# Performance work log

Measured on AMD Instinct MI355X. Metric: run time of the kernel, lower is better.

Reference implementation:

```python
import jax, jax.numpy as jnp
import numpy as np

N, IN_DIM, D, H, E_DIM, G, NPG = 512, 16, 256, 8, 6, 32, 16
C = D           # per-head channels in GATv2Conv/TransformerConv (out_channels=d_model)
HD = D // H     # MultiheadAttention head dim


def _ln(x, g, b, eps=1e-5):
    m = jnp.mean(x, -1, keepdims=True)
    v = jnp.mean((x - m) ** 2, -1, keepdims=True)
    return (x - m) * jax.lax.rsqrt(v + eps) * g + b


def _seg_softmax(logits, seg, n):
    # numerically stable softmax over edges grouped by destination node
    m = jax.ops.segment_max(logits, seg, num_segments=n)
    m = jnp.where(jnp.isfinite(m), m, 0.0)
    e = jnp.exp(logits - m[seg])
    s = jax.ops.segment_sum(e, seg, num_segments=n)
    return e / jnp.maximum(s[seg], 1e-16)


def _forward(x, edge_attr, emb_w, emb_b, emb_g, emb_bb, pe, gat_lw, gat_lb, gat_rw, gat_rb, gat_ew, gat_att, gat_bias, tq_w, tq_b, tk_w, tk_b, tv_w, tv_b, te_w, tskip_w, tskip_b, tbeta_w, ln_g, ln_b, mha_in_w, mha_in_b, mha_out_w, mha_out_b, pool_w, pool_b, c1_w, c1_b, c1_g, c1_bb, rb_w, rb_b, rb_g, rb_bb, c2_w, c2_b, edge_index, batch):
    src, dst = edge_index[0], edge_index[1]
    E = edge_attr.shape[0]
    # input embedding (Linear + LayerNorm) + learned positional encoding (eval: no dropout)
    h = _ln(x @ emb_w.T + emb_b, emb_g, emb_bb) + pe[:N]
    residual = h
    # --- GATv2Conv(d_model, d_model, heads=H, edge_dim=6, concat=False, add_self_loops=False) ---
    xl = (h @ gat_lw.T + gat_lb).reshape(N, H, C)          # source transform
    xr = (h @ gat_rw.T + gat_rb).reshape(N, H, C)          # target transform
    ee = (edge_attr @ gat_ew.T).reshape(E, H, C)
    z = jax.nn.leaky_relu(xl[src] + xr[dst] + ee, 0.2)
    a = _seg_softmax(jnp.einsum('ehc,hc->eh', z, gat_att), dst, N)
    x_gat = jax.ops.segment_sum(xl[src] * a[..., None], dst, num_segments=N).mean(1) + gat_bias
    x_gat = _ln(x_gat, ln_g, ln_b)
    # --- TransformerConv(d_model, d_model, heads=H, edge_dim=6, concat=False, beta=True) ---
    te = (edge_attr @ te_w.T).reshape(E, H, C)
    q = (x_gat @ tq_w.T + tq_b).reshape(N, H, C)[dst]
    k = (x_gat @ tk_w.T + tk_b).reshape(N, H, C)[src] + te
    v = (x_gat @ tv_w.T + tv_b).reshape(N, H, C)[src] + te
    a2 = _seg_softmax((q * k).sum(-1) / np.sqrt(C).astype(np.float32), dst, N)
    out = jax.ops.segment_sum(v * a2[..., None], dst, num_segments=N).mean(1)
    r = x_gat @ tskip_w.T + tskip_b
    beta = jax.nn.sigmoid(jnp.concatenate([out, r, out - r], -1) @ tbeta_w.T)
    x_tr = _ln(beta * r + (1.0 - beta) * out, ln_g, ln_b)
    # --- dynamic attention mask: after the repeat/permute/reshape gymnastics this equals
    #     ds[:N] repeated H*N times, reshaped to [H, N, N] ---
    im = edge_attr[:, 5]
    ds = jnp.exp(-0.5 * ((im - 125.09) / 15.0) ** 2)
    ds = 1.0 - (ds - ds.min()) / (ds.max() - ds.min())
    mask = jnp.repeat(ds[:N], H * N).reshape(H, N, N)
    # --- cross MultiheadAttention (query=x_tr, key=x_gat, value=h, attn_mask added) ---
    wq, wk, wv = jnp.split(mha_in_w, 3, axis=0)
    bq, bk, bv = jnp.split(mha_in_b, 3, axis=0)
    qh = ((x_tr @ wq.T + bq) / np.sqrt(HD).astype(np.float32)).reshape(N, H, HD).transpose(1, 0, 2)
    kh = (x_gat @ wk.T + bk).reshape(N, H, HD).transpose(1, 0, 2)
    vh = (h @ wv.T + bv).reshape(N, H, HD).transpose(1, 0, 2)
    attn = jax.nn.softmax(qh @ kh.transpose(0, 2, 1) + mask, axis=-1)   # [H,N,N]
    o = (attn @ vh).transpose(1, 0, 2).reshape(N, D) @ mha_out_w.T + mha_out_b
    # torch broadcast of [N,1,D] attn output + [N,D] residual -> [N,N,D]
    x3 = o[:, None, :] + residual[None, :, :]
    # attention pooling: softmax over a size-1 dim yields all-ones scores (kept faithfully)
    x2 = x3.reshape(N * N, D)
    brep = jnp.tile(batch, N)
    score = jax.nn.softmax(x2 @ pool_w.T + pool_b, axis=1)
    pooled = jax.ops.segment_sum(score * x2, brep, num_segments=G)
    # classifier: Linear->LN->GELU->ResidualBlockv2->Linear (dropout off in eval)
    c = jax.nn.gelu(_ln(pooled @ c1_w.T + c1_b, c1_g, c1_bb), approximate=False)
    c = c + jax.nn.gelu(_ln(c @ rb_w.T + rb_b, rb_g, rb_bb), approximate=False)
    return c @ c2_w.T + c2_b   # [G, 1]


def setup_inputs():
    key = jax.random.key(0)
    ks = iter(jax.random.split(key, 64))
    f = lambda *sh: 0.02 * jax.random.normal(next(ks), sh, jnp.float32)
    # G fully-connected directed cliques of NPG nodes (no self loops) -> every node has in-edges
    i = np.arange(NPG)
    s, t = np.meshgrid(i, i, indexing='ij')
    msk = s != t
    s, t = s[msk], t[msk]
    off = (np.arange(G) * NPG)[:, None]
    edge_index = jnp.asarray(np.stack([(s[None] + off).reshape(-1), (t[None] + off).reshape(-1)]), jnp.int32)
    E = edge_index.shape[1]
    batch = jnp.asarray(np.repeat(np.arange(G), NPG), jnp.int32)
    x = jax.random.normal(next(ks), (N, IN_DIM), jnp.float32)
    edge_attr = jax.random.normal(next(ks), (E, E_DIM), jnp.float32)
    edge_attr = edge_attr.at[:, 5].set(edge_attr[:, 5] * 30.0 + 125.0)  # invariant-mass-like column
    HC = H * C
    return dict(
        x=x, edge_attr=edge_attr,
        emb_w=f(D, IN_DIM), emb_b=f(D), emb_g=jnp.ones(D), emb_bb=jnp.zeros(D),
        pe=f(1000, D),
        gat_lw=f(HC, D), gat_lb=f(HC), gat_rw=f(HC, D), gat_rb=f(HC),
        gat_ew=f(HC, E_DIM), gat_att=f(H, C), gat_bias=f(C),
        tq_w=f(HC, D), tq_b=f(HC), tk_w=f(HC, D), tk_b=f(HC),
        tv_w=f(HC, D), tv_b=f(HC), te_w=f(HC, E_DIM),
        tskip_w=f(D, D), tskip_b=f(D), tbeta_w=f(1, 3 * D),
        ln_g=jnp.ones(D), ln_b=jnp.zeros(D),
        mha_in_w=f(3 * D, D), mha_in_b=f(3 * D), mha_out_w=f(D, D), mha_out_b=f(D),
        pool_w=f(1, D), pool_b=f(1),
        c1_w=f(128, D), c1_b=f(128), c1_g=jnp.ones(128), c1_bb=jnp.zeros(128),
        rb_w=f(128, 128), rb_b=f(128), rb_g=jnp.ones(128), rb_bb=jnp.zeros(128),
        c2_w=f(1, 128), c2_b=f(1),
        edge_index=edge_index, batch=batch)


def reference(x, edge_attr, emb_w, emb_b, emb_g, emb_bb, pe, gat_lw, gat_lb, gat_rw, gat_rb, gat_ew, gat_att, gat_bias, tq_w, tq_b, tk_w, tk_b, tv_w, tv_b, te_w, tskip_w, tskip_b, tbeta_w, ln_g, ln_b, mha_in_w, mha_in_b, mha_out_w, mha_out_b, pool_w, pool_b, c1_w, c1_b, c1_g, c1_bb, rb_w, rb_b, rb_g, rb_bb, c2_w, c2_b, edge_index, batch):
    return _forward(x, edge_attr, emb_w, emb_b, emb_g, emb_bb, pe, gat_lw, gat_lb, gat_rw, gat_rb, gat_ew, gat_att, gat_bias, tq_w, tq_b, tk_w, tk_b, tv_w, tv_b, te_w, tskip_w, tskip_b, tbeta_w, ln_g, ln_b, mha_in_w, mha_in_b, mha_out_w, mha_out_b, pool_w, pool_b, c1_w, c1_b, c1_g, c1_bb, rb_w, rb_b, rb_g, rb_bb, c2_w, c2_b, edge_index, batch)
```

## Files before the change

kernel.cpp:

```cpp
#include <hip/hip_runtime.h>
#include <hip/hip_bf16.h>
#include <math.h>

#define NN 512
#define DM 256
#define NH 8
#define NG 32
#define NPG 16
#define INDIM 16
#define BIGW (2048 * 256)
#define WT_SKIP 0
#define WT_MHA  65536
#define WT_OUT  (65536 + 196608)
#define WT_TOTAL (65536 + 196608 + 65536)

typedef __hip_bfloat16 bf16;
typedef __attribute__((ext_vector_type(8))) short short8;
typedef __attribute__((ext_vector_type(4))) float f32x4;

__device__ __forceinline__ float b2f(bf16 v) { return __bfloat162float(v); }
__device__ __forceinline__ bf16 f2b(float v) { return __float2bfloat16(v); }
__device__ __forceinline__ short f2bs(float v) { bf16 t = __float2bfloat16(v); return *(short*)&t; }
__device__ __forceinline__ float fin(float v) {
    return (v == v && v > -1e30f && v < 1e30f) ? v : 0.f;
}
__device__ __forceinline__ int is_bf16(const void* ones_arr) {
    return ((const unsigned short*)ones_arr)[0] == 0x3F80u;
}
__device__ __forceinline__ float ldv(const void* p, size_t i, int bf) {
    return bf ? b2f(((const bf16*)p)[i]) : ((const float*)p)[i];
}

__device__ __forceinline__ void unpack8(uint4 u, float* w) {
    unsigned uu[4] = {u.x, u.y, u.z, u.w};
    #pragma unroll
    for (int j = 0; j < 4; j++) {
        __hip_bfloat162 b2 = *reinterpret_cast<const __hip_bfloat162*>(&uu[j]);
        float2 f = __bfloat1622float2(b2);
        w[2 * j] = f.x; w[2 * j + 1] = f.y;
    }
}
__device__ __forceinline__ float4 bload4(const bf16* p) {
    uint2 u = *(const uint2*)p;
    __hip_bfloat162 a = *reinterpret_cast<const __hip_bfloat162*>(&u.x);
    __hip_bfloat162 b = *reinterpret_cast<const __hip_bfloat162*>(&u.y);
    float2 f0 = __bfloat1622float2(a), f1 = __bfloat1622float2(b);
    return make_float4(f0.x, f0.y, f1.x, f1.y);
}

__device__ __forceinline__ float dot256(const float* xrow, const bf16* wrow) {
    const uint4* w4 = (const uint4*)wrow;
    uint4 q = w4[0];
    float acc = 0.f;
    for (int k8 = 0; k8 < 32; k8++) {
        uint4 qn = w4[(k8 + 1) & 31];
        float w[8]; unpack8(q, w);
        const float4* sp = (const float4*)&xrow[k8 * 8];
        float4 a0 = sp[0], a1 = sp[1];
        acc += a0.x*w[0] + a0.y*w[1] + a0.z*w[2] + a0.w*w[3]
             + a1.x*w[4] + a1.y*w[5] + a1.z*w[6] + a1.w*w[7];
        q = qn;
    }
    return acc;
}

__device__ __forceinline__ float dot256T(const float* xrow, const bf16* wt, int r) {
    float acc = 0.f;
    #pragma unroll 8
    for (int k4 = 0; k4 < 64; k4++) {
        uint2 u = *(const uint2*)(wt + ((size_t)k4 * 256 + r) * 4);
        __hip_bfloat162 b0 = *reinterpret_cast<const __hip_bfloat162*>(&u.x);
        __hip_bfloat162 b1 = *reinterpret_cast<const __hip_bfloat162*>(&u.y);
        float2 f0 = __bfloat1622float2(b0), f1 = __bfloat1622float2(b1);
        float4 xv = *(const float4*)&xrow[k4 * 4];
        acc += xv.x * f0.x + xv.y * f0.y + xv.z * f1.x + xv.w * f1.y;
    }
    return acc;
}

template<int BS>
__device__ __forceinline__ float ln_norm(float v, float g, float b, float* red) {
    int t = threadIdx.x;
    red[t] = v; __syncthreads();
    for (int s = BS / 2; s > 0; s >>= 1) { if (t < s) red[t] += red[t + s]; __syncthreads(); }
    float mean = red[0] * (1.0f / (float)BS); __syncthreads();
    float d = v - mean;
    red[t] = d * d; __syncthreads();
    for (int s = BS / 2; s > 0; s >>= 1) { if (t < s) red[t] += red[t + s]; __syncthreads(); }
    float var = red[0] * (1.0f / (float)BS); __syncthreads();
    return d * rsqrtf(var + 1e-5f) * g + b;
}

struct CvtTab { const void* p[35]; int cum[36]; };
struct Cvt5 { const void* p[5]; };
__global__ void k_convert_all(Cvt5 tab5, CvtTab tab, const void* ones, bf16* wbig,
                              bf16* wbuf, float* gz, int nz, bf16* wt,
                              float* pre1, float* pre2, float* h) {
    int i = blockIdx.x * 256 + threadIdx.x;
    int a = blockIdx.y;
    int bf = is_bf16(ones);
    if (a < 5) {
        if (i >= BIGW) return;
        float v = bf ? b2f(((const bf16*)tab5.p[a])[i]) : ((const float*)tab5.p[a])[i];
        int row = i >> 8, k = i & 255;
        int hh = row >> 8, col = row & 255;
        int T = col >> 4, n16 = col & 15;
        int ks = k >> 5, quad = (k >> 3) & 3, j = k & 7;
        int dst = ((((hh * 16 + T) * 8 + ks) * 4 + quad) * 16 + n16) * 8 + j;
        wbig[(size_t)a * BIGW + dst] = f2b(v);
    } else if (a == 5) {
        if (i < tab.cum[35]) {
            int aa = 0;
            while (i >= tab.cum[aa + 1]) aa++;
            wbuf[i] = f2b(ldv(tab.p[aa], i - tab.cum[aa], bf));
        } else if (i < tab.cum[35] + nz) {
            gz[i - tab.cum[35]] = 0.f;
        } else if (i < tab.cum[35] + nz + WT_TOTAL) {
            int off = i - tab.cum[35] - nz;
            if (off < 65536) {
                int row = off >> 8, k = off & 255;
                wt[WT_SKIP + ((k >> 2) * 256 + row) * 4 + (k & 3)] =
                    f2b(ldv(tab.p[16], off, bf));
            } else if (off < 65536 + 196608) {
                int o2 = off - 65536;
                int row = o2 >> 8, k = o2 & 255;
                int which = row >> 8, r = row & 255;
                wt[WT_MHA + which * 65536 + ((k >> 2) * 256 + r) * 4 + (k & 3)] =
                    f2b(ldv(tab.p[21], o2, bf));
            } else {
                int o2 = off - 65536 - 196608;
                int row = o2 >> 8, k = o2 & 255;
                wt[WT_OUT + ((k >> 2) * 256 + row) * 4 + (k & 3)] =
                    f2b(ldv(tab.p[23], o2, bf));
            }
        }
    } else {
        int n = blockIdx.x;
        if (n >= NN) return;
        int t = threadIdx.x;
        size_t gi = (size_t)n * DM + t;
        pre1[gi] = 0.f;
        pre2[gi] = 0.f;
        __shared__ float xin[INDIM];
        __shared__ float red[DM];
        if (t < INDIM) xin[t] = ldv(tab.p[0], n * INDIM + t, bf);
        __syncthreads();
        float acc = ldv(tab.p[3], t, bf);
        #pragma unroll
        for (int k = 0; k < INDIM; k++) acc += xin[k] * ldv(tab.p[2], t * INDIM + k, bf);
        float y = ln_norm<DM>(acc, ldv(tab.p[4], t, bf), ldv(tab.p[5], t, bf), red);
        h[gi] = fin(y + ldv(tab.p[6], gi, bf));
    }
}

__device__ __forceinline__ void row_softmax16(float* M, int tid) {
    if (tid < NPG) {
        float* row = M + tid * NPG;
        float m = -1e30f;
        #pragma unroll
        for (int s = 0; s < NPG; s++) m = fmaxf(m, row[s]);
        if (m < -1e29f) {
            #pragma unroll
            for (int s = 0; s < NPG; s++) row[s] = 0.f;
        } else {
            float sum = 0.f;
            #pragma unroll
            for (int s = 0; s < NPG; s++) sum += expf(row[s] - m);
            float inv = 1.f / fmaxf(sum, 1e-16f);
            #pragma unroll
            for (int s = 0; s < NPG; s++) row[s] = expf(row[s] - m) * inv;
        }
    }
}

__global__ __launch_bounds__(512, 1)
void k_gat_fused(const float* h, const bf16* lw, const bf16* rw,
                 const bf16* lb, const bf16* rbv, const bf16* eww, const bf16* attw,
                 const bf16* ea, const int* src, const int* dst, int epg, float* pre) {
    extern __shared__ char smraw[];
    int g = blockIdx.x, hh = blockIdx.y, tid = threadIdx.x;
    bf16* hb     = (bf16*)smraw;
    bf16* ew_s   = hb + NPG * DM;
    bf16* att_s  = ew_s + 6 * DM;
    float* ea_s  = (float*)(att_s + DM);
    float* Mx    = ea_s + 6 * epg;
    int* sl_s    = (int*)(Mx + NPG * NPG);
    int* dl_s    = sl_s + epg;
    bf16* xl_s   = (bf16*)(dl_s + epg);
    bf16* xr_s   = xl_s + NPG * DM;

    int ebase = g * epg;
    for (int i = tid; i < NPG * DM; i += 512) hb[i] = f2b(h[(size_t)g * NPG * DM + i]);
    for (int i = tid; i < 6 * DM; i += 512) {
        int f = i >> 8, cc = i & 255;
        ew_s[f * DM + cc] = eww[(size_t)(hh * DM + cc) * 6 + f];
    }
    if (tid < DM) att_s[tid] = attw[hh * DM + tid];
    for (int i = tid; i < 6 * epg; i += 512) {
        int f = i / epg, e = i - f * epg;
        ea_s[f * epg + e] = b2f(ea[(size_t)(ebase + e) * 6 + f]);
    }
    if (tid < NPG * NPG) Mx[tid] = -1e30f;
    if (tid < epg) {
        int e = ebase + tid;
        sl_s[tid] = (src[e] - g * NPG) & (NPG - 1);
        dl_s[tid] = (dst[e] - g * NPG) & (NPG - 1);
    }
    __syncthreads();

    int lane = tid & 63, wave = tid >> 6;
    int n16 = lane & 15, quad = lane >> 4;
    f32x4 accA[2], accB[2];
    #pragma unroll
    for (int ct = 0; ct < 2; ct++) { accA[ct] = (f32x4)0.f; accB[ct] = (f32x4)0.f; }
    for (int ks = 0; ks < 8; ks++) {
        short8 a8 = *(const short8*)&hb[n16 * DM + ks * 32 + quad * 8];
        #pragma unroll
        for (int ct = 0; ct < 2; ct++) {
            int T = ct * 8 + wave;
            size_t fo = (((size_t)(hh * 16 + T) * 8 + ks) * 4 + quad) * 128 + n16 * 8;
            short8 bL = *(const short8*)(lw + fo);
            short8 bR = *(const short8*)(rw + fo);
            accA[ct] = __builtin_amdgcn_mfma_f32_16x16x32_bf16(a8, bL, accA[ct], 0, 0, 0);
            accB[ct] = __builtin_amdgcn_mfma_f32_16x16x32_bf16(a8, bR, accB[ct], 0, 0, 0);
        }
    }
    #pragma unroll
    for (int ct = 0; ct < 2; ct++) {
        int col = (ct * 8 + wave) * 16 + n16;
        float blv = b2f(lb[hh * DM + col]), brv = b2f(rbv[hh * DM + col]);
        #pragma unroll
        for (int reg = 0; reg < 4; reg++) {
            int row = quad * 4 + reg;
            xl_s[row * DM + col] = f2b(accA[ct][reg] + blv);
            xr_s[row * DM + col] = f2b(accB[ct][reg] + brv);
        }
    }
    __syncthreads();

    int c4 = lane * 4;
    for (int ei = wave; ei < epg; ei += 8) {
        int sl = sl_s[ei], dl = dl_s[ei];
        float ee0 = 0.f, ee1 = 0.f, ee2 = 0.f, ee3 = 0.f;
        #pragma unroll
        for (int f = 0; f < 6; f++) {
            float eb = ea_s[f * epg + ei];
            float4 wf = bload4(&ew_s[f * DM + c4]);
            ee0 += eb * wf.x; ee1 += eb * wf.y; ee2 += eb * wf.z; ee3 += eb * wf.w;
        }
        float4 av = bload4(&att_s[c4]);
        float4 xlv = bload4(&xl_s[sl * DM + c4]);
        float4 xrv = bload4(&xr_s[dl * DM + c4]);
        float z0 = xlv.x + xrv.x + ee0;
        float z1 = xlv.y + xrv.y + ee1;
        float z2 = xlv.z + xrv.z + ee2;
        float z3 = xlv.w + xrv.w + ee3;
        z0 = (z0 >= 0.f) ? z0 : 0.2f * z0;
        z1 = (z1 >= 0.f) ? z1 : 0.2f * z1;
        z2 = (z2 >= 0.f) ? z2 : 0.2f * z2;
        z3 = (z3 >= 0.f) ? z3 : 0.2f * z3;
        float acc = z0 * av.x + z1 * av.y + z2 * av.z + z3 * av.w;
        #pragma unroll
        for (int off = 32; off > 0; off >>= 1) acc += __shfl_down(acc, off);
        if (lane == 0) Mx[dl * NPG + sl] = fin(acc);
    }
    __syncthreads();
    row_softmax16(Mx, tid);
    __syncthreads();

    int c = tid & 255, halfd = tid >> 8;
    float xlv[NPG];
    #pragma unroll
    for (int s = 0; s < NPG; s++) xlv[s] = b2f(xl_s[s * DM + c]);
    #pragma unroll
    for (int dd = 0; dd < 8; dd++) {
        int d = halfd * 8 + dd;
        const float* Ar = Mx + d * NPG;
        float acc = 0.f;
        #pragma unroll
        for (int s = 0; s < NPG; s++) acc += Ar[s] * xlv[s];
        atomicAdd(&pre[(size_t)(g * NPG + d) * DM + c], fin(acc));
    }
}

__global__ void k_gat_post_skip(const float* pre, const bf16* gat_bias, const bf16* lng,
                                const bf16* lnb, const bf16* wt, const bf16* skb,
                                float* x_gat, float* rbuf) {
    int n = blockIdx.x, t = threadIdx.x;
    __shared__ float red[DM];
    __shared__ float xrow[DM];
    float v = pre[(size_t)n * DM + t] * 0.125f + b2f(gat_bias[t]);
    float y = fin(ln_norm<DM>(v, b2f(lng[t]), b2f(lnb[t]), red));
    x_gat[(size_t)n * DM + t] = y;
    xrow[t] = y;
    __syncthreads();
    rbuf[(size_t)n * DM + t] = fin(dot256T(xrow, wt + WT_SKIP, t) + b2f(skb[t]));
}

__global__ __launch_bounds__(512, 1)
void k_tr_fused(const float* xg, const bf16* qw, const bf16* kw, const bf16* vw,
                const bf16* qb, const bf16* kb, const bf16* vb, const bf16* tew,
                const bf16* ea, const int* src, const int* dst, int epg, float* pre) {
    extern __shared__ char smraw[];
    int g = blockIdx.x, hh = blockIdx.y, tid = threadIdx.x;
    bf16* hb    = (bf16*)smraw;
    bf16* tw_s  = hb + NPG * DM;
    float* ea_s = (float*)(tw_s + 6 * DM);
    float* Lqk  = ea_s + 6 * epg;
    float* Mx   = Lqk + NPG * NPG;
    float* P    = Mx + NPG * NPG;
    float* W6   = P + NPG * 6;
    int* emap   = (int*)(W6 + NPG * 6);
    int* sl_s   = emap + NPG * NPG;
    int* dl_s   = sl_s + epg;
    bf16* q_s   = (bf16*)(dl_s + epg);
    bf16* k_s   = q_s + NPG * DM;
    bf16* v_s   = k_s + NPG * DM;

    int ebase = g * epg;
    for (int i = tid; i < NPG * DM; i += 512) hb[i] = f2b(xg[(size_t)g * NPG * DM + i]);
    for (int i = tid; i < 6 * DM; i += 512) {
        int f = i >> 8, cc = i & 255;
        tw_s[f * DM + cc] = tew[(size_t)(hh * DM + cc) * 6 + f];
    }
    for (int i = tid; i < 6 * epg; i += 512) {
        int f = i / epg, e = i - f * epg;
        ea_s[f * epg + e] = b2f(ea[(size_t)(ebase + e) * 6 + f]);
    }
    if (tid < NPG * NPG) { Mx[tid] = -1e30f; emap[tid] = -1; }
    if (tid < epg) {
        int e = ebase + tid;
        sl_s[tid] = (src[e] - g * NPG) & (NPG - 1);
        dl_s[tid] = (dst[e] - g * NPG) & (NPG - 1);
    }
    __syncthreads();

    int lane = tid & 63, wave = tid >> 6;
    int n16 = lane & 15, quad = lane >> 4;
    f32x4 aQ[2], aK[2], aV[2];
    #pragma unroll
    for (int ct = 0; ct < 2; ct++) { aQ[ct] = (f32x4)0.f; aK[ct] = (f32x4)0.f; aV[ct] = (f32x4)0.f; }
    for (int ks = 0; ks < 8; ks++) {
        short8 a8 = *(const short8*)&hb[n16 * DM + ks * 32 + quad * 8];
        #pragma unroll
        for (int ct = 0; ct < 2; ct++) {
            int T = ct * 8 + wave;
            size_t fo = (((size_t)(hh * 16 + T) * 8 + ks) * 4 + quad) * 128 + n16 * 8;
            short8 bQ = *(const short8*)(qw + fo);
            short8 bK = *(const short8*)(kw + fo);
            short8 bV = *(const short8*)(vw + fo);
            aQ[ct] = __builtin_amdgcn_mfma_f32_16x16x32_bf16(a8, bQ, aQ[ct], 0, 0, 0);
            aK[ct] = __builtin_amdgcn_mfma_f32_16x16x32_bf16(a8, bK, aK[ct], 0, 0, 0);
            aV[ct] = __builtin_amdgcn_mfma_f32_16x16x32_bf16(a8, bV, aV[ct], 0, 0, 0);
        }
    }
    #pragma unroll
    for (int ct = 0; ct < 2; ct++) {
        int col = (ct * 8 + wave) * 16 + n16;
        float bq = b2f(qb[hh * DM + col]), bk = b2f(kb[hh * DM + col]), bv = b2f(vb[hh * DM + col]);
        #pragma unroll
        for (int reg = 0; reg < 4; reg++) {
            int row = quad * 4 + reg;
            q_s[row * DM + col] = f2b(aQ[ct][reg] + bq);
            k_s[row * DM + col] = f2b(aK[ct][reg] + bk);
            v_s[row * DM + col] = f2b(aV[ct][reg] + bv);
        }
    }
    __syncthreads();

    if (wave == 0) {
        f32x4 acc = (f32x4)0.f;
        for (int ks = 0; ks < 8; ks++) {
            short8 a8 = *(const short8*)&q_s[n16 * DM + ks * 32 + quad * 8];
            short8 b8 = *(const short8*)&k_s[n16 * DM + ks * 32 + quad * 8];
            acc = __builtin_amdgcn_mfma_f32_16x16x32_bf16(a8, b8, acc, 0, 0, 0);
        }
        #pragma unroll
        for (int reg = 0; reg < 4; reg++)
            Lqk[(quad * 4 + reg) * NPG + n16] = acc[reg];
    } else if (wave <= 2) {
        int idx = tid - 64;
        if (idx < NPG * 6) {
            int d = idx / 6, f = idx - d * 6;
            const bf16* qr = q_s + d * DM;
            const bf16* twr = tw_s + f * DM;
            float acc = 0.f;
            for (int cc = 0; cc < DM; cc += 4) {
                float4 qv = bload4(qr + cc);
                float4 t4 = bload4(twr + cc);
                acc += qv.x * t4.x + qv.y * t4.y + qv.z * t4.z + qv.w * t4.w;
            }
            P[idx] = acc;
        }
    }
    __syncthreads();

    if (tid < epg) {
        int sl = sl_s[tid], dl = dl_s[tid];
        float acc = Lqk[dl * NPG + sl];
        #pragma unroll
        for (int f = 0; f < 6; f++) acc += ea_s[f * epg + tid] * P[dl * 6 + f];
        Mx[dl * NPG + sl] = fin(acc * 0.0625f);
        emap[dl * NPG + sl] = tid;
    }
    __syncthreads();
    row_softmax16(Mx, tid);
    __syncthreads();
    if (tid < NPG * 6) {
        int d = tid / 6, f = tid - d * 6;
        float acc = 0.f;
        #pragma unroll
        for (int s = 0; s < NPG; s++) {
            int e = emap[d * NPG + s];
            if (e >= 0) acc += Mx[d * NPG + s] * ea_s[f * epg + e];
        }
        W6[tid] = acc;
    }
    __syncthreads();

    int c = tid & 255, halfd = tid >> 8;
    float vv[NPG];
    #pragma unroll
    for (int s = 0; s < NPG; s++) vv[s] = b2f(v_s[s * DM + c]);
    float twc[6];
    #pragma unroll
    for (int f = 0; f < 6; f++) twc[f] = b2f(tw_s[f * DM + c]);
    #pragma unroll
    for (int dd = 0; dd < 8; dd++) {
        int d = halfd * 8 + dd;
        const float* Ar = Mx + d * NPG;
        const float* Wr = W6 + d * 6;
        float acc = 0.f;
        #pragma unroll
        for (int s = 0; s < NPG; s++) acc += Ar[s] * vv[s];
        #pragma unroll
        for (int f = 0; f < 6; f++) acc += Wr[f] * twc[f];
        atomicAdd(&pre[(size_t)(g * NPG + d) * DM + c], fin(acc));
    }
}

__global__ void k_tr_post_qkv(const float* pre, const float* rbuf, const float* x_gat,
                              const float* h, const bf16* tbeta, const bf16* lng,
                              const bf16* lnb, const bf16* wt, const bf16* mb, float* qkv) {
    int n = blockIdx.x, t = threadIdx.x;
    __shared__ float red[DM];
    __shared__ float xtr_s[DM];
    __shared__ float xg_s[DM];
    __shared__ float h_s[DM];
    __shared__ float beta_sh;
    float outc = pre[(size_t)n * DM + t] * 0.125f;
    float rc = rbuf[(size_t)n * DM + t];
    xg_s[t] = x_gat[(size_t)n * DM + t];
    h_s[t] = h[(size_t)n * DM + t];
    float w1 = b2f(tbeta[t]), w2 = b2f(tbeta[DM + t]), w3 = b2f(tbeta[2 * DM + t]);
    red[t] = outc * (w1 + w3) + rc * (w2 - w3);
    __syncthreads();
    for (int s2 = 128; s2 > 0; s2 >>= 1) { if (t < s2) red[t] += red[t + s2]; __syncthreads(); }
    if (t == 0) beta_sh = 1.0f / (1.0f + expf(-red[0]));
    __syncthreads();
    float beta = beta_sh;
    float mix = beta * rc + (1.0f - beta) * outc;
    float y = fin(ln_norm<DM>(mix, b2f(lng[t]), b2f(lnb[t]), red));
    xtr_s[t] = y;
    __syncthreads();
    float q = (dot256T(xtr_s, wt + WT_MHA, t) + b2f(mb[t])) * 0.17677669529663689f;
    float k = dot256T(xg_s, wt + WT_MHA + 65536, t) + b2f(mb[DM + t]);
    float v = dot256T(h_s, wt + WT_MHA + 131072, t) + b2f(mb[2 * DM + t]);
    qkv[(size_t)n * DM + t] = fin(q);
    qkv[((size_t)NN + n) * DM + t] = fin(k);
    qkv[((size_t)2 * NN + n) * DM + t] = fin(v);
}

#define SPAD 516
__global__ __launch_bounds__(256, 1)
void k_attn(const float* qh, const float* kh, const float* vh, float* ao) {
    extern __shared__ char sm[];
    bf16* KF   = (bf16*)sm;
    float* Sc  = (float*)(KF + 8192);
    float* Op  = Sc + 16 * SPAD;
    float* red = Op + 4 * 16 * 32;
    int qt = blockIdx.x, hd = blockIdx.y, tid = threadIdx.x;
    int lane = tid & 63, wave = tid >> 6, n16 = lane & 15, quad = lane >> 4;

    short8 a8q;
    {
        const float* qp = &qh[(size_t)(qt * 16 + n16) * DM + hd * 32 + quad * 8];
        float4 q0 = *(const float4*)qp, q1 = *((const float4*)qp + 1);
        a8q[0] = f2bs(q0.x); a8q[1] = f2bs(q0.y); a8q[2] = f2bs(q0.z); a8q[3] = f2bs(q0.w);
        a8q[4] = f2bs(q1.x); a8q[5] = f2bs(q1.y); a8q[6] = f2bs(q1.z); a8q[7] = f2bs(q1.w);
    }

    for (int half = 0; half < 2; half++) {
        __syncthreads();
        for (int i = tid; i < 8192; i += 256) {
            int jj = i >> 5, d = i & 31;
            bf16 val = f2b(kh[(size_t)(half * 256 + jj) * DM + hd * 32 + d]);
            int ktl = jj >> 4, nn = jj & 15, qd = d >> 3, j8 = d & 7;
            KF[((ktl * 4 + qd) * 16 + nn) * 8 + j8] = val;
        }
        __syncthreads();
        #pragma unroll
        for (int it = 0; it < 4; it++) {
            int ktl = wave * 4 + it;
            short8 b8 = *(const short8*)&KF[((ktl * 4 + quad) * 16 + n16) * 8];
            f32x4 acc = (f32x4)0.f;
            acc = __builtin_amdgcn_mfma_f32_16x16x32_bf16(a8q, b8, acc, 0, 0, 0);
            #pragma unroll
            for (int reg = 0; reg < 4; reg++)
                Sc[(quad * 4 + reg) * SPAD + half * 256 + ktl * 16 + n16] = acc[reg];
        }
    }
    __syncthreads();

    int r = tid >> 4, li = tid & 15;
    float m = -1e30f;
    for (int s = 0; s < 32; s++) m = fmaxf(m, Sc[r * SPAD + li + 16 * s]);
    red[r * 16 + li] = m; __syncthreads();
    for (int st = 8; st > 0; st >>= 1) {
        if (li < st) red[r * 16 + li] = fmaxf(red[r * 16 + li], red[r * 16 + li + st]);
        __syncthreads();
    }
    m = red[r * 16];
    __syncthreads();
    float sum = 0.f;
    for (int s = 0; s < 32; s++) sum += expf(Sc[r * SPAD + li + 16 * s] - m);
    red[r * 16 + li] = sum; __syncthreads();
    for (int st = 8; st > 0; st >>= 1) {
        if (li < st) red[r * 16 + li] += red[r * 16 + li + st];
        __syncthreads();
    }
    float inv = 1.0f / fmaxf(red[r * 16], 1e-16f);
    for (int s = 0; s < 32; s++) {
        int idx = r * SPAD + li + 16 * s;
        Sc[idx] = expf(Sc[idx] - m) * inv;
    }

    f32x4 o0 = (f32x4)0.f, o1 = (f32x4)0.f;
    for (int half = 0; half < 2; half++) {
        __syncthreads();
        for (int i = tid; i < 8192; i += 256) {
            int jj = i >> 5, d = i & 31;
            bf16 val = f2b(vh[(size_t)(half * 256 + jj) * DM + hd * 32 + d]);
            int ksl = jj >> 5, kin = jj & 31, qd = kin >> 3, j8 = kin & 7;
            int nn = d & 15, which = d >> 4;
            KF[which * 4096 + ((ksl * 4 + qd) * 16 + nn) * 8 + j8] = val;
        }
        __syncthreads();
        #pragma unroll
        for (int it = 0; it < 2; it++) {
            int ksl = wave * 2 + it;
            int ks = half * 8 + ksl;
            const float* sp = &Sc[n16 * SPAD + ks * 32 + quad * 8];
            float4 s0 = *(const float4*)sp, s1 = *((const float4*)sp + 1);
            short8 a8;
            a8[0] = f2bs(s0.x); a8[1] = f2bs(s0.y); a8[2] = f2bs(s0.z); a8[3] = f2bs(s0.w);
            a8[4] = f2bs(s1.x); a8[5] = f2bs(s1.y); a8[6] = f2bs(s1.z); a8[7] = f2bs(s1.w);
            short8 bv0 = *(const short8*)&KF[((ksl * 4 + quad) * 16 + n16) * 8];
            short8 bv1 = *(const short8*)&KF[4096 + ((ksl * 4 + quad) * 16 + n16) * 8];
            o0 = __builtin_amdgcn_mfma_f32_16x16x32_bf16(a8, bv0, o0, 0, 0, 0);
            o1 = __builtin_amdgcn_mfma_f32_16x16x32_bf16(a8, bv1, o1, 0, 0, 0);
        }
    }
    #pragma unroll
    for (int reg = 0; reg < 4; reg++) {
        Op[wave * 512 + (quad * 4 + reg) * 32 + n16] = o0[reg];
        Op[wave * 512 + (quad * 4 + reg) * 32 + 16 + n16] = o1[reg];
    }
    __syncthreads();
    for (int e = tid; e < 512; e += 256) {
        float v = Op[e] + Op[512 + e] + Op[1024 + e] + Op[1536 + e];
        ao[(size_t)(qt * 16 + (e >> 5)) * DM + hd * 32 + (e & 31)] = fin(v);
    }
}

__global__ void k_outproj(const float* ao, const bf16* wt, const bf16* B,
                          float* obuf, float* gsum_o) {
    int n = blockIdx.x, t = threadIdx.x;
    __shared__ float xrow[DM];
    xrow[t] = ao[(size_t)n * DM + t];
    __syncthreads();
    float v = fin(dot256T(xrow, wt + WT_OUT, t) + b2f(B[t]));
    obuf[(size_t)n * DM + t] = v;
    atomicAdd(&gsum_o[(n >> 4) * DM + t], v);
}

__global__ void k_mlp(const float* gsum_o, const float* h,
                      const bf16* c1_w, const bf16* c1_b, const bf16* c1_g,
                      const bf16* c1_bb, const bf16* rb_w, const bf16* rb_b,
                      const bf16* rb_g, const bf16* rb_bb, const bf16* c2_w,
                      const bf16* c2_b, const void* ones, void* out) {
    int g = blockIdx.x, t = threadIdx.x;
    __shared__ float pl[DM];
    __shared__ float u[128];
    __shared__ float red[128];
    float os0 = 0.f, os1 = 0.f, hs0 = 0.f, hs1 = 0.f;
    #pragma unroll
    for (int b = 0; b < NG; b++) {
        os0 += gsum_o[b * DM + t];
        os1 += gsum_o[b * DM + t + 128];
    }
    #pragma unroll
    for (int j = 0; j < NPG; j++) {
        hs0 += h[(size_t)(g * NPG + j) * DM + t];
        hs1 += h[(size_t)(g * NPG + j) * DM + t + 128];
    }
    pl[t]       = fin((float)NPG * os0 + (float)NN * hs0);
    pl[t + 128] = fin((float)NPG * os1 + (float)NN * hs1);
    __syncthreads();
    float acc = dot256(pl, c1_w + (size_t)t * DM) + b2f(c1_b[t]);
    float y = ln_norm<128>(acc, b2f(c1_g[t]), b2f(c1_bb[t]), red);
    float gl = 0.5f * y * (1.0f + erff(y * 0.70710678118654752f));
    u[t] = gl; __syncthreads();
    float acc2 = b2f(rb_b[t]);
    for (int k = 0; k < 128; k++) acc2 += u[k] * b2f(rb_w[(size_t)t * 128 + k]);
    float y2 = ln_norm<128>(acc2, b2f(rb_g[t]), b2f(rb_bb[t]), red);
    float cfin = gl + 0.5f * y2 * (1.0f + erff(y2 * 0.70710678118654752f));
    red[t] = cfin * b2f(c2_w[t]);
    __syncthreads();
    for (int s2 = 64; s2 > 0; s2 >>= 1) { if (t < s2) red[t] += red[t + s2]; __syncthreads(); }
    if (t == 0) {
        float res = fin(red[0] + b2f(c2_b[0]));
        if (is_bf16(ones)) ((bf16*)out)[g] = f2b(res);
        else               ((float*)out)[g] = res;
    }
}

extern "C" void kernel_launch(void* const* d_in, const int* in_sizes, int n_in,
                              void* d_out, int out_size, void* d_ws, size_t ws_size,
                              hipStream_t stream) {
    const int E = in_sizes[1] / 6;
    const int epg = E / NG;
    const int* eidx = (const int*)d_in[42];
    const int* srcp = eidx;
    const int* dstp = eidx + E;
    const void* ones = d_in[4];

    static const int idxs[35] = {0,1,2,3,4,5,6,8,10,11,12,13,15,17,19,20,21,22,23,24,
                                 25,26,27,28,29,32,33,34,35,36,37,38,39,40,41};
    CvtTab tab;
    int wOff[44];
    int cum = 0;
    for (int a = 0; a < 35; a++) {
        tab.p[a] = d_in[idxs[a]];
        tab.cum[a] = cum;
        wOff[idxs[a]] = cum;
        cum += in_sizes[idxs[a]];
    }
    tab.cum[35] = cum;
    const int totalW = cum;
    Cvt5 tab5;
    tab5.p[0] = d_in[7];  tab5.p[1] = d_in[9];
    tab5.p[2] = d_in[14]; tab5.p[3] = d_in[16]; tab5.p[4] = d_in[18];

    bf16* wbuf = (bf16*)d_ws;
    size_t wbytes = ((size_t)totalW * 2 + 255) & ~(size_t)255;
    float* fb = (float*)((char*)d_ws + wbytes);
    const size_t SL = (size_t)NN * DM;
    float* h      = fb;
    float* x_gat  = fb + SL;
    float* rbuf   = fb + 2 * SL;
    float* pre1   = fb + 3 * SL;
    float* pre2   = fb + 4 * SL;
    float* qkv    = fb + 5 * SL;
    float* gsum_o = fb + 8 * SL;
    bf16* wt      = (bf16*)(gsum_o + NG * DM);
    bf16* wbig = (bf16*)qkv;
    float* ao = pre1;
    float* obuf = pre2;
    const int NZ = NG * DM;

    #define WB(i) (wbuf + wOff[i])

    int need5 = totalW + NZ + WT_TOTAL;
    int gx = BIGW / 256;
    if ((need5 + 255) / 256 > gx) gx = (need5 + 255) / 256;
    k_convert_all<<<dim3(gx, 7), 256, 0, stream>>>(tab5, tab, ones, wbig, wbuf,
                                                   gsum_o, NZ, wt, pre1, pre2, h);

    int gat_lds = NPG*DM*2 + 6*DM*2 + DM*2 + (6*epg + NPG*NPG + 2*epg) * 4
                + 2*NPG*DM*2 + 16;
    k_gat_fused<<<dim3(NG, NH), 512, gat_lds, stream>>>(
        h, wbig, wbig + BIGW, WB(8), WB(10), WB(11), WB(12), WB(1), srcp, dstp, epg, pre1);
    k_gat_post_skip<<<NN, DM, 0, stream>>>(pre1, WB(13), WB(24), WB(25), wt, WB(22),
                                           x_gat, rbuf);

    int tr_lds = NPG*DM*2 + 6*DM*2 + (6*epg + 2*NPG*NPG + 2*NPG*6) * 4
               + (NPG*NPG + 2*epg) * 4 + 3*NPG*DM*2 + 16;
    k_tr_fused<<<dim3(NG, NH), 512, tr_lds, stream>>>(
        x_gat, wbig + 2 * (size_t)BIGW, wbig + 3 * (size_t)BIGW, wbig + 4 * (size_t)BIGW,
        WB(15), WB(17), WB(19), WB(20), WB(1), srcp, dstp, epg, pre2);
    k_tr_post_qkv<<<NN, DM, 0, stream>>>(pre2, rbuf, x_gat, h, WB(23), WB(24), WB(25),
                                         wt, WB(27), qkv);

    int attn_lds = 8192 * 2 + (16 * SPAD + 4 * 16 * 32 + 16 * 16) * 4;
    k_attn<<<dim3(NN / 16, NH), 256, attn_lds, stream>>>(qkv, qkv + SL, qkv + 2 * SL, ao);
    k_outproj<<<NN, DM, 0, stream>>>(ao, wt, WB(29), obuf, gsum_o);

    k_mlp<<<NG, 128, 0, stream>>>(gsum_o, h, WB(32), WB(33), WB(34), WB(35),
                                  WB(36), WB(37), WB(38), WB(39), WB(40), WB(41),
                                  ones, d_out);
    #undef WB
}
```

Measured before the change: 272.7 us.

## Fuse GAT post-LN into transformer kernel and fold out-projection into pooled MLP

Removes the k_gat_post_skip launch by computing the GAT bias+LayerNorm inside k_tr_fused, with head 0 writing x_gat, and moves the skip projection into k_tr_post_qkv. It also drops k_outproj: since only the graph-summed output projection is consumed, attention rows are reduced into a single 256-vector and the out-projection is applied once in k_mlp using linearity. This cuts two kernel launches and intermediate buffers. The cost is that all 8 head blocks recompute the LayerNorm redundantly.

```diff
diff --git a/kernel.cpp b/kernel.cpp
--- a/kernel.cpp
+++ b/kernel.cpp
@@ -283,24 +283,12 @@
     }
 }
 
-__global__ void k_gat_post_skip(const float* pre, const bf16* gat_bias, const bf16* lng,
-                                const bf16* lnb, const bf16* wt, const bf16* skb,
-                                float* x_gat, float* rbuf) {
-    int n = blockIdx.x, t = threadIdx.x;
-    __shared__ float red[DM];
-    __shared__ float xrow[DM];
-    float v = pre[(size_t)n * DM + t] * 0.125f + b2f(gat_bias[t]);
-    float y = fin(ln_norm<DM>(v, b2f(lng[t]), b2f(lnb[t]), red));
-    x_gat[(size_t)n * DM + t] = y;
-    xrow[t] = y;
-    __syncthreads();
-    rbuf[(size_t)n * DM + t] = fin(dot256T(xrow, wt + WT_SKIP, t) + b2f(skb[t]));
-}
-
 __global__ __launch_bounds__(512, 1)
-void k_tr_fused(const float* xg, const bf16* qw, const bf16* kw, const bf16* vw,
+void k_tr_fused(const float* pre1, const bf16* gbias, const bf16* lng, const bf16* lnb,
+                const bf16* qw, const bf16* kw, const bf16* vw,
                 const bf16* qb, const bf16* kb, const bf16* vb, const bf16* tew,
-                const bf16* ea, const int* src, const int* dst, int epg, float* pre) {
+                const bf16* ea, const int* src, const int* dst, int epg,
+                float* x_gat, float* pre) {
     extern __shared__ char smraw[];
     int g = blockIdx.x, hh = blockIdx.y, tid = threadIdx.x;
     bf16* hb    = (bf16*)smraw;
@@ -316,9 +304,12 @@
     bf16* q_s   = (bf16*)(dl_s + epg);
     bf16* k_s   = q_s + NPG * DM;
     bf16* v_s   = k_s + NPG * DM;
+    float* red2 = (float*)(v_s + NPG * DM);
+    float* mst  = red2 + NPG * 32;
+    float* rst  = mst + NPG;
 
     int ebase = g * epg;
-    for (int i = tid; i < NPG * DM; i += 512) hb[i] = f2b(xg[(size_t)g * NPG * DM + i]);
+    const float* pg = pre1 + (size_t)g * NPG * DM;
     for (int i = tid; i < 6 * DM; i += 512) {
         int f = i >> 8, cc = i & 255;
         tw_s[f * DM + cc] = tew[(size_t)(hh * DM + cc) * 6 + f];
@@ -332,6 +323,49 @@
         int e = ebase + tid;
         sl_s[tid] = (src[e] - g * NPG) & (NPG - 1);
         dl_s[tid] = (dst[e] - g * NPG) & (NPG - 1);
+    }
+
+    int li = tid & 31, rr = tid >> 5;
+    float part = 0.f;
+    #pragma unroll
+    for (int k = 0; k < 8; k++) {
+        int cc = li + 32 * k;
+        part += pg[rr * DM + cc] * 0.125f + b2f(gbias[cc]);
+    }
+    red2[rr * 32 + li] = part; __syncthreads();
+    for (int st = 16; st > 0; st >>= 1) {
+        if (li < st) red2[rr * 32 + li] += red2[rr * 32 + li + st];
+        __syncthreads();
+    }
+    float mean = red2[rr * 32] * (1.0f / 256.0f);
+    __syncthreads();
+    float vpart = 0.f;
+    #pragma unroll
+    for (int k = 0; k < 8; k++) {
+        int cc = li + 32 * k;
+        float d = pg[rr * DM + cc] * 0.125f + b2f(gbias[cc]) - mean;
+        vpart += d * d;
+    }
+    red2[rr * 32 + li] = vpart; __syncthreads();
+    for (int st = 16; st > 0; st >>= 1) {
+        if (li < st) red2[rr * 32 + li] += red2[rr * 32 + li + st];
+        __syncthreads();
+    }
+    if (li == 0) {
+        mst[rr] = mean;
+        rst[rr] = rsqrtf(red2[rr * 32] * (1.0f / 256.0f) + 1e-5f);
+    }
+    __syncthreads();
+    {
+        int c = tid & 255, hd2 = tid >> 8;
+        #pragma unroll
+        for (int dd = 0; dd < 8; dd++) {
+            int row = hd2 * 8 + dd;
+            float v = pg[row * DM + c] * 0.125f + b2f(gbias[c]);
+            float y = fin((v - mst[row]) * rst[row] * b2f(lng[c]) + b2f(lnb[c]));
+            hb[row * DM + c] = f2b(y);
+            if (hh == 0) x_gat[(size_t)(g * NPG + row) * DM + c] = y;
+        }
     }
     __syncthreads();
 
@@ -439,9 +473,10 @@
     }
 }
 
-__global__ void k_tr_post_qkv(const float* pre, const float* rbuf, const float* x_gat,
+__global__ void k_tr_post_qkv(const float* pre, const float* x_gat,
                               const float* h, const bf16* tbeta, const bf16* lng,
-                              const bf16* lnb, const bf16* wt, const bf16* mb, float* qkv) {
+                              const bf16* lnb, const bf16* wt, const bf16* skb,
+                              const bf16* mb, float* qkv) {
     int n = blockIdx.x, t = threadIdx.x;
     __shared__ float red[DM];
     __shared__ float xtr_s[DM];
@@ -449,9 +484,10 @@
     __shared__ float h_s[DM];
     __shared__ float beta_sh;
     float outc = pre[(size_t)n * DM + t] * 0.125f;
-    float rc = rbuf[(size_t)n * DM + t];
     xg_s[t] = x_gat[(size_t)n * DM + t];
     h_s[t] = h[(size_t)n * DM + t];
+    __syncthreads();
+    float rc = fin(dot256T(xg_s, wt + WT_SKIP, t) + b2f(skb[t]));
     float w1 = b2f(tbeta[t]), w2 = b2f(tbeta[DM + t]), w3 = b2f(tbeta[2 * DM + t]);
     red[t] = outc * (w1 + w3) + rc * (w2 - w3);
     __syncthreads();
@@ -473,7 +509,7 @@
 
 #define SPAD 516
 __global__ __launch_bounds__(256, 1)
-void k_attn(const float* qh, const float* kh, const float* vh, float* ao) {
+void k_attn(const float* qh, const float* kh, const float* vh, float* aosum) {
     extern __shared__ char sm[];
     bf16* KF   = (bf16*)sm;
     float* Sc  = (float*)(KF + 8192);
@@ -567,43 +603,38 @@
         Op[wave * 512 + (quad * 4 + reg) * 32 + 16 + n16] = o1[reg];
     }
     __syncthreads();
-    for (int e = tid; e < 512; e += 256) {
-        float v = Op[e] + Op[512 + e] + Op[1024 + e] + Op[1536 + e];
-        ao[(size_t)(qt * 16 + (e >> 5)) * DM + hd * 32 + (e & 31)] = fin(v);
-    }
-}
-
-__global__ void k_outproj(const float* ao, const bf16* wt, const bf16* B,
-                          float* obuf, float* gsum_o) {
-    int n = blockIdx.x, t = threadIdx.x;
-    __shared__ float xrow[DM];
-    xrow[t] = ao[(size_t)n * DM + t];
-    __syncthreads();
-    float v = fin(dot256T(xrow, wt + WT_OUT, t) + b2f(B[t]));
-    obuf[(size_t)n * DM + t] = v;
-    atomicAdd(&gsum_o[(n >> 4) * DM + t], v);
-}
-
-__global__ void k_mlp(const float* gsum_o, const float* h,
+    for (int e = tid; e < 512; e += 256)
+        Op[e] = Op[e] + Op[512 + e] + Op[1024 + e] + Op[1536 + e];
+    __syncthreads();
+    if (tid < 32) {
+        float s = 0.f;
+        #pragma unroll
+        for (int row = 0; row < 16; row++) s += Op[row * 32 + tid];
+        atomicAdd(&aosum[hd * 32 + tid], fin(s));
+    }
+}
+
+__global__ void k_mlp(const float* aosum, const float* h, const bf16* wt, const bf16* outb,
                       const bf16* c1_w, const bf16* c1_b, const bf16* c1_g,
                       const bf16* c1_bb, const bf16* rb_w, const bf16* rb_b,
                       const bf16* rb_g, const bf16* rb_bb, const bf16* c2_w,
                       const bf16* c2_b, const void* ones, void* out) {
     int g = blockIdx.x, t = threadIdx.x;
+    __shared__ float as[DM];
     __shared__ float pl[DM];
     __shared__ float u[128];
     __shared__ float red[128];
-    float os0 = 0.f, os1 = 0.f, hs0 = 0.f, hs1 = 0.f;
-    #pragma unroll
-    for (int b = 0; b < NG; b++) {
-        os0 += gsum_o[b * DM + t];
-        os1 += gsum_o[b * DM + t + 128];
-    }
+    as[t] = aosum[t];
+    as[t + 128] = aosum[t + 128];
+    float hs0 = 0.f, hs1 = 0.f;
     #pragma unroll
     for (int j = 0; j < NPG; j++) {
         hs0 += h[(size_t)(g * NPG + j) * DM + t];
         hs1 += h[(size_t)(g * NPG + j) * DM + t + 128];
     }
+    __syncthreads();
+    float os0 = dot256T(as, wt + WT_OUT, t) + (float)NN * b2f(outb[t]);
+    float os1 = dot256T(as, wt + WT_OUT, t + 128) + (float)NN * b2f(outb[t + 128]);
     pl[t]       = fin((float)NPG * os0 + (float)NN * hs0);
     pl[t + 128] = fin((float)NPG * os1 + (float)NN * hs1);
     __syncthreads();
@@ -658,16 +689,13 @@
     const size_t SL = (size_t)NN * DM;
     float* h      = fb;
     float* x_gat  = fb + SL;
-    float* rbuf   = fb + 2 * SL;
-    float* pre1   = fb + 3 * SL;
-    float* pre2   = fb + 4 * SL;
-    float* qkv    = fb + 5 * SL;
-    float* gsum_o = fb + 8 * SL;
-    bf16* wt      = (bf16*)(gsum_o + NG * DM);
+    float* pre1   = fb + 2 * SL;
+    float* pre2   = fb + 3 * SL;
+    float* qkv    = fb + 4 * SL;
+    float* aosum  = fb + 7 * SL;
+    bf16* wt      = (bf16*)(aosum + DM);
     bf16* wbig = (bf16*)qkv;
-    float* ao = pre1;
-    float* obuf = pre2;
-    const int NZ = NG * DM;
+    const int NZ = DM;
 
     #define WB(i) (wbuf + wOff[i])
 
@@ -675,28 +703,26 @@
     int gx = BIGW / 256;
     if ((need5 + 255) / 256 > gx) gx = (need5 + 255) / 256;
     k_convert_all<<<dim3(gx, 7), 256, 0, stream>>>(tab5, tab, ones, wbig, wbuf,
-                                                   gsum_o, NZ, wt, pre1, pre2, h);
+                                                   aosum, NZ, wt, pre1, pre2, h);
 
     int gat_lds = NPG*DM*2 + 6*DM*2 + DM*2 + (6*epg + NPG*NPG + 2*epg) * 4
                 + 2*NPG*DM*2 + 16;
     k_gat_fused<<<dim3(NG, NH), 512, gat_lds, stream>>>(
         h, wbig, wbig + BIGW, WB(8), WB(10), WB(11), WB(12), WB(1), srcp, dstp, epg, pre1);
-    k_gat_post_skip<<<NN, DM, 0, stream>>>(pre1, WB(13), WB(24), WB(25), wt, WB(22),
-                                           x_gat, rbuf);
 
     int tr_lds = NPG*DM*2 + 6*DM*2 + (6*epg + 2*NPG*NPG + 2*NPG*6) * 4
-               + (NPG*NPG + 2*epg) * 4 + 3*NPG*DM*2 + 16;
+               + (NPG*NPG + 2*epg) * 4 + 3*NPG*DM*2 + (NPG*32 + 2*NPG) * 4 + 16;
     k_tr_fused<<<dim3(NG, NH), 512, tr_lds, stream>>>(
-        x_gat, wbig + 2 * (size_t)BIGW, wbig + 3 * (size_t)BIGW, wbig + 4 * (size_t)BIGW,
-        WB(15), WB(17), WB(19), WB(20), WB(1), srcp, dstp, epg, pre2);
-    k_tr_post_qkv<<<NN, DM, 0, stream>>>(pre2, rbuf, x_gat, h, WB(23), WB(24), WB(25),
-                                         wt, WB(27), qkv);
+        pre1, WB(13), WB(24), WB(25),
+        wbig + 2 * (size_t)BIGW, wbig + 3 * (size_t)BIGW, wbig + 4 * (size_t)BIGW,
+        WB(15), WB(17), WB(19), WB(20), WB(1), srcp, dstp, epg, x_gat, pre2);
+    k_tr_post_qkv<<<NN, DM, 0, stream>>>(pre2, x_gat, h, WB(23), WB(24), WB(25),
+                                         wt, WB(22), WB(27), qkv);
 
     int attn_lds = 8192 * 2 + (16 * SPAD + 4 * 16 * 32 + 16 * 16) * 4;
-    k_attn<<<dim3(NN / 16, NH), 256, attn_lds, stream>>>(qkv, qkv + SL, qkv + 2 * SL, ao);
-    k_outproj<<<NN, DM, 0, stream>>>(ao, wt, WB(29), obuf, gsum_o);
-
-    k_mlp<<<NG, 128, 0, stream>>>(gsum_o, h, WB(32), WB(33), WB(34), WB(35),
+    k_attn<<<dim3(NN / 16, NH), 256, attn_lds, stream>>>(qkv, qkv + SL, qkv + 2 * SL, aosum);
+
+    k_mlp<<<NG, 128, 0, stream>>>(aosum, h, wt, WB(29), WB(32), WB(33), WB(34), WB(35),
                                   WB(36), WB(37), WB(38), WB(39), WB(40), WB(41),
                                   ones, d_out);
     #undef WB
```

Result: no change. 272.6 us (-0.0%).
